# Kernel tuning notes

Hardware: AMD Instinct MI355X
Metric: run time of the kernel (lower is better)

The kernel has to match this reference:

```python
import jax, jax.numpy as jnp
import numpy as np

NUM_HEAD = 2
KR = 3          # kernel_range = [3, 3]
SHIFT = 1
N_P = KR * KR   # 9 taps
PAD = (KR // 2) * SHIFT  # 1
OFFSETS = [(i, j) for i in (-(KR // 2), 0, KR // 2) if True for j in ()]  # placeholder, real list below
OFFSETS = [(i, j) for i in range(-(KR // 2), KR // 2 + 1) for j in range(-(KR // 2), KR // 2 + 1)]


def _conv3x3(x, w, b):
    # x: [B,H,W,Cin], w: [3,3,Cin,Cout] -> SAME conv + bias
    y = jax.lax.conv_general_dilated(
        x, w, window_strides=(1, 1), padding='SAME',
        dimension_numbers=('NHWC', 'HWIO', 'NHWC'))
    return y + b


def setup_inputs() -> dict:
    key = jax.random.key(0)
    B, H, W, D = 4, 128, 128, 64
    ks = jax.random.split(key, 10)
    sc = 0.05  # small init like glorot
    return {
        'x': jax.random.normal(ks[0], (B, H, W, D), jnp.float32),
        # 1x1 conv kernels stored as matrices (equiv. to (1,1,Cin,Cout))
        'K_P': jax.random.normal(ks[1], (D, D * N_P), jnp.float32) * sc,
        'V_P': jax.random.normal(ks[2], (D, D * N_P), jnp.float32) * sc,
        'Q_P': jax.random.normal(ks[3], (D, D), jnp.float32) * sc,
        'ff1_kernel': jax.random.normal(ks[4], (D, D), jnp.float32) * sc,
        'ff1_bias': jax.random.normal(ks[5], (D,), jnp.float32) * sc,
        'ff2_kernel': jax.random.normal(ks[6], (3, 3, D, 2 * D), jnp.float32) * sc,
        'ff2_bias': jax.random.normal(ks[7], (2 * D,), jnp.float32) * sc,
        'ff3_kernel': jax.random.normal(ks[8], (3, 3, 2 * D, D), jnp.float32) * sc,
        'ff3_bias': jax.random.normal(ks[9], (D,), jnp.float32) * sc,
    }


def reference(x, K_P, V_P, Q_P, ff1_kernel, ff1_bias, ff2_kernel, ff2_bias,
              ff3_kernel, ff3_bias):
    B, H, W, D = x.shape
    hd = D // NUM_HEAD

    # 1x1 projections; K/V produce N_P channel chunks, one per tap
    x_k = jnp.einsum('bhwd,de->bhwe', x, K_P).reshape(B, H, W, N_P, D)
    x_v = jnp.einsum('bhwd,de->bhwe', x, V_P).reshape(B, H, W, N_P, D)
    x_q = jnp.einsum('bhwd,de->bhwe', x, Q_P)

    pad5 = ((0, 0), (PAD, PAD), (PAD, PAD), (0, 0), (0, 0))
    k_pad = jnp.pad(x_k, pad5)
    v_pad = jnp.pad(x_v, pad5)

    # tap t uses channel chunk t at spatial offset OFFSETS[t]*SHIFT
    def taps(padded):
        return jnp.stack(
            [padded[:, PAD + i * SHIFT:PAD + i * SHIFT + H,
                    PAD + j * SHIFT:PAD + j * SHIFT + W, t, :]
             for t, (i, j) in enumerate(OFFSETS)], axis=3)  # [B,H,W,N_P,D]

    k_taps = taps(k_pad)
    v_taps = taps(v_pad)

    # validity mask (padded taps get score 0 before softmax, as in original)
    m_pad = jnp.pad(jnp.ones((B, H, W), x.dtype), ((0, 0), (PAD, PAD), (PAD, PAD)))
    mask = jnp.stack(
        [m_pad[:, PAD + i * SHIFT:PAD + i * SHIFT + H,
               PAD + j * SHIFT:PAD + j * SHIFT + W]
         for (i, j) in OFFSETS], axis=3)  # [B,H,W,N_P]

    kh = k_taps.reshape(B, H, W, N_P, NUM_HEAD, hd)
    vh = v_taps.reshape(B, H, W, N_P, NUM_HEAD, hd)
    qh = x_q.reshape(B, H, W, NUM_HEAD, hd)

    # scores per head over taps; masked-multiply then /3, as in original
    scores = jnp.einsum('bhwtnc,bhwnc->bhwnt', kh, qh)
    scores = scores * mask[:, :, :, None, :] / 3.0
    alpha = jax.nn.softmax(scores, axis=-1)  # over taps
    attn = jnp.einsum('bhwnt,bhwtnc->bhwnc', alpha, vh).reshape(B, H, W, D)

    # FFN: 1x1 conv -> relu -> 3x3 conv -> relu -> 3x3 conv -> relu
    t = jax.nn.relu(jnp.einsum('bhwd,de->bhwe', attn, ff1_kernel) + ff1_bias)
    t = jax.nn.relu(_conv3x3(t, ff2_kernel, ff2_bias))
    t = jax.nn.relu(_conv3x3(t, ff3_kernel, ff3_bias))
    return t
```

## Files before the change

### kernel.cpp

```cpp
#include <hip/hip_runtime.h>


typedef _Float16 half8 __attribute__((ext_vector_type(8)));
typedef float f32x4 __attribute__((ext_vector_type(4)));

#define PLANE 524288

__device__ __forceinline__ f32x4 mfma16(half8 a, half8 b, f32x4 c) {
  return __builtin_amdgcn_mfma_f32_16x16x32_f16(a, b, c, 0, 0, 0);
}
__device__ __forceinline__ half8 ldfrag(const _Float16* p) { return *(const half8*)p; }
__device__ __forceinline__ half8 zfrag() { half8 z = {}; return z; }

__device__ __forceinline__ void gload_lds16(const _Float16* g, _Float16* l) {
  __builtin_amdgcn_global_load_lds(
      (const __attribute__((address_space(1))) void*)g,
      (__attribute__((address_space(3))) void*)l, 16, 0, 0);
}

__global__ __launch_bounds__(256) void prep(
    const float* __restrict__ x, const float* __restrict__ Kp,
    const float* __restrict__ Vp, const float* __restrict__ Qp,
    const float* __restrict__ W1, const float* __restrict__ F2,
    const float* __restrict__ F3, _Float16* __restrict__ xh,
    _Float16* __restrict__ out) {
  if (blockIdx.x < 2048) {
    const int t = threadIdx.x;
    const int px = blockIdx.x * 32 + (t >> 3);
    const int oct = t & 7;
    const float4* s = (const float4*)(x + (size_t)px * 64 + oct * 8);
    float4 a = s[0], b = s[1];
    half8 h = { (_Float16)a.x, (_Float16)a.y, (_Float16)a.z, (_Float16)a.w,
                (_Float16)b.x, (_Float16)b.y, (_Float16)b.z, (_Float16)b.w };
    *(half8*)(xh + (size_t)oct * PLANE + (size_t)px * 8) = h;
    return;
  }
  int e = (blockIdx.x - 2048) * 256 + threadIdx.x;
  int j = e & 7, l = (e >> 3) & 63, f = e >> 9;
  int l15 = l & 15, q8 = (l >> 4) * 8;
  float v;
  if (f < 8)        { int mb = f >> 1, kb = f & 1;
                      v = Qp[(kb*32 + q8 + j) * 64 + mb*16 + l15]; }
  else if (f < 80)  { int g = f - 8, t = g >> 3, mb = (g >> 1) & 3, kb = g & 1;
                      v = Kp[(kb*32 + q8 + j) * 576 + t*64 + mb*16 + l15]; }
  else if (f < 152) { int g = f - 80, t = g >> 3, kb = (g >> 2) & 1, nb = g & 3;
                      v = Vp[(kb*32 + q8 + j) * 576 + t*64 + nb*16 + l15]; }
  else if (f < 160) { int g = f - 152, kb = g >> 2, nb = g & 3;
                      v = W1[(kb*32 + q8 + j) * 64 + nb*16 + l15]; }
  else if (f < 304) { int g = f - 160, t = g >> 4, kb = (g >> 3) & 1, nb = g & 7;
                      v = F2[(t*64 + kb*32 + q8 + j) * 128 + nb*16 + l15]; }
  else              { int g = f - 304, t = g >> 4, kb = (g >> 2) & 3, nb = g & 3;
                      v = F3[(t*128 + kb*32 + q8 + j) * 64 + nb*16 + l15]; }
  out[e] = (_Float16)v;
}

__global__ __launch_bounds__(512) void attn_ff1(
    const _Float16* __restrict__ xh, const _Float16* __restrict__ wf,
    const float* __restrict__ f1b, _Float16* __restrict__ t1g) {
  extern __shared__ _Float16 smem[];
  const int lane = threadIdx.x & 63, wid = threadIdx.x >> 6;
  const int l15 = lane & 15, q8 = (lane >> 4) * 8;
  const int row = blockIdx.x * 2 + (wid >> 2);
  const int rw = wid & 3;
  const int p0 = row * 128 + rw * 32;
  const int h = row & 127;
  const int w0 = rw * 32;
  const int oct0 = lane >> 4;
  float* dent = (float*)(smem + 77824) + wid * 64;

  {
    const _Float16* gw = wf + 4096 + (size_t)(wid * 19) * 512;
    _Float16* lw = smem + wid * 19 * 512;
    for (int i = 0; i < 19; ++i)
      gload_lds16(gw + i * 512 + lane * 8, lw + i * 512);
  }

  half8 ax0[2], ax1[2];
#pragma unroll
  for (int m = 0; m < 2; ++m) {
    const size_t px = (size_t)(p0 + m * 16 + l15);
    ax0[m] = ldfrag(xh + (size_t)oct0 * PLANE + px * 8);
    ax1[m] = ldfrag(xh + (size_t)(oct0 + 4) * PLANE + px * 8);
  }
  f32x4 qT[2][4];
#pragma unroll
  for (int cb = 0; cb < 4; ++cb) {
    half8 aq0 = ldfrag(wf + (cb * 2 + 0) * 512 + lane * 8);
    half8 aq1 = ldfrag(wf + (cb * 2 + 1) * 512 + lane * 8);
#pragma unroll
    for (int m = 0; m < 2; ++m) {
      f32x4 c = {};
      c = mfma16(aq0, ax0[m], c);
      c = mfma16(aq1, ax1[m], c);
      qT[m][cb] = c;
    }
  }

  auto load_tap = [&](int t, half8 (&x0)[2], half8 (&x1)[2]) {
    const int dh = t / 3 - 1, dw = t % 3 - 1;
    const bool rk = (unsigned)(h + dh) < 128u;
#pragma unroll
    for (int m = 0; m < 2; ++m) {
      const bool cv = rk && ((unsigned)(w0 + m * 16 + l15 + dw) < 128u);
      const size_t px = (size_t)(p0 + m * 16 + l15 + dh * 128 + dw);
      x0[m] = cv ? ldfrag(xh + (size_t)oct0 * PLANE + px * 8) : zfrag();
      x1[m] = cv ? ldfrag(xh + (size_t)(oct0 + 4) * PLANE + px * 8) : zfrag();
    }
  };

  float den0[2] = {0.f, 0.f}, den1[2] = {0.f, 0.f};
  auto score_tap = [&](int t, half8 (&x0)[2], half8 (&x1)[2],
                       float (&e0)[2], float (&e1)[2]) {
    const int dh = t / 3 - 1;
    const bool rowok = (unsigned)(h + dh) < 128u;
    half8 kf[8];
    if (rowok) {
#pragma unroll
      for (int f = 0; f < 8; ++f)
        kf[f] = ldfrag(smem + (t * 8 + f) * 512 + lane * 8);
    }
#pragma unroll
    for (int m = 0; m < 2; ++m) {
      float pa = 0.f, pb = 0.f;
      if (rowok) {
#pragma unroll
        for (int cb = 0; cb < 4; ++cb) {
          f32x4 c = {};
          c = mfma16(kf[cb * 2 + 0], x0[m], c);
          c = mfma16(kf[cb * 2 + 1], x1[m], c);
          float d = qT[m][cb].x * c.x + qT[m][cb].y * c.y
                  + qT[m][cb].z * c.z + qT[m][cb].w * c.w;
          if (cb < 2) pa += d; else pb += d;
        }
        pa += __shfl_xor(pa, 16, 64); pa += __shfl_xor(pa, 32, 64);
        pb += __shfl_xor(pb, 16, 64); pb += __shfl_xor(pb, 32, 64);
      }
      e0[m] = __expf(pa * (1.f / 3.f));
      e1[m] = __expf(pb * (1.f / 3.f));
      den0[m] += e0[m]; den1[m] += e1[m];
    }
  };

  half8 q0[4][2], q1[4][2];
  load_tap(0, q0[0], q1[0]);
  load_tap(1, q0[1], q1[1]);
  load_tap(2, q0[2], q1[2]);

  __syncthreads();

  float e0c[2], e1c[2];
  score_tap(0, q0[0], q1[0], e0c, e1c);

  const _Float16* BVl = smem + 36864;
  f32x4 at[2][4];
#pragma unroll
  for (int m = 0; m < 2; ++m)
#pragma unroll
    for (int nb = 0; nb < 4; ++nb) at[m][nb] = f32x4{};

#pragma unroll
  for (int t = 0; t < 9; ++t) {
    if (t + 3 < 9) load_tap(t + 3, q0[(t + 3) & 3], q1[(t + 3) & 3]);
    const bool rowok = (unsigned)(h + (t / 3 - 1)) < 128u;
    if (rowok) {
      half8 vf[8];
#pragma unroll
      for (int f = 0; f < 8; ++f) vf[f] = ldfrag(BVl + (t * 8 + f) * 512 + lane * 8);
#pragma unroll
      for (int m = 0; m < 2; ++m) {
        _Float16 h0 = (_Float16)e0c[m], h1 = (_Float16)e1c[m];
        half8 b0 = {h0, h0, h0, h0, h0, h0, h0, h0};
        half8 b1 = {h1, h1, h1, h1, h1, h1, h1, h1};
        half8 s00 = q0[t & 3][m] * b0, s01 = q1[t & 3][m] * b0;
        half8 s10 = q0[t & 3][m] * b1, s11 = q1[t & 3][m] * b1;
#pragma unroll
        for (int nb = 0; nb < 2; ++nb) {
          at[m][nb]     = mfma16(s00, vf[0 * 4 + nb],     at[m][nb]);
          at[m][nb]     = mfma16(s01, vf[1 * 4 + nb],     at[m][nb]);
          at[m][nb + 2] = mfma16(s10, vf[0 * 4 + nb + 2], at[m][nb + 2]);
          at[m][nb + 2] = mfma16(s11, vf[1 * 4 + nb + 2], at[m][nb + 2]);
        }
      }
    }
    if (t < 8) {
      float e0n[2], e1n[2];
      score_tap(t + 1, q0[(t + 1) & 3], q1[(t + 1) & 3], e0n, e1n);
#pragma unroll
      for (int m = 0; m < 2; ++m) { e0c[m] = e0n[m]; e1c[m] = e1n[m]; }
    }
  }

#pragma unroll
  for (int m = 0; m < 2; ++m) {
    dent[(m * 2 + 0) * 16 + l15] = den0[m];
    dent[(m * 2 + 1) * 16 + l15] = den1[m];
  }
  f32x4 iv[2][2];
#pragma unroll
  for (int m = 0; m < 2; ++m)
#pragma unroll
    for (int hd = 0; hd < 2; ++hd) {
      f32x4 dv = *(const f32x4*)(dent + (m * 2 + hd) * 16 + (lane >> 4) * 4);
      iv[m][hd] = f32x4{1.f / dv.x, 1.f / dv.y, 1.f / dv.z, 1.f / dv.w};
    }

  __syncthreads();
  _Float16* myt = smem + wid * 2304;
#pragma unroll
  for (int m = 0; m < 2; ++m)
#pragma unroll
    for (int nb = 0; nb < 4; ++nb) {
      const int hd = nb >> 1;
#pragma unroll
      for (int r = 0; r < 4; ++r)
        myt[m * 1152 + ((lane >> 4) * 4 + r) * 72 + nb * 16 + l15] =
            (_Float16)(at[m][nb][r] * iv[m][hd][r]);
    }
  const _Float16* B1l = smem + 73728;
  const int pxl = lane >> 2;
  const int co0 = lane & 3;
#pragma unroll
  for (int m = 0; m < 2; ++m) {
    _Float16* T = myt + m * 1152;
    half8 aa0 = ldfrag(T + l15 * 72 + q8);
    half8 aa1 = ldfrag(T + l15 * 72 + 32 + q8);
#pragma unroll
    for (int nb = 0; nb < 4; ++nb) {
      f32x4 c = {};
      c = mfma16(aa0, ldfrag(B1l + (0 * 4 + nb) * 512 + lane * 8), c);
      c = mfma16(aa1, ldfrag(B1l + (1 * 4 + nb) * 512 + lane * 8), c);
      float bv = f1b[nb * 16 + l15];
#pragma unroll
      for (int r = 0; r < 4; ++r)
        T[((lane >> 4) * 4 + r) * 72 + nb * 16 + l15] =
            (_Float16)fmaxf(c[r] + bv, 0.f);
    }
    const size_t pxg = (size_t)(p0 + m * 16 + pxl);
    half8 h0 = ldfrag(T + pxl * 72 + co0 * 8);
    half8 h1 = ldfrag(T + pxl * 72 + (co0 + 4) * 8);
    *(half8*)(t1g + (size_t)co0 * PLANE + pxg * 8) = h0;
    *(half8*)(t1g + (size_t)(co0 + 4) * PLANE + pxg * 8) = h1;
  }
}

template <int KB, int NBL, int COUT, int DEPTH>
__global__ __launch_bounds__(512, 4) void conv3x3(
    const _Float16* __restrict__ in, const _Float16* __restrict__ wfrag,
    const float* __restrict__ bias, void* __restrict__ outp, int out_fp32) {
  extern __shared__ _Float16 smem[];
  constexpr int NS = DEPTH + 1;
  const int lane = threadIdx.x & 63, wid = threadIdx.x >> 6;
  const int l15 = lane & 15;
  const int nh = blockIdx.x & 1;
  const int pairIdx = blockIdx.x >> 1;
  const int row = pairIdx * 2 + (wid >> 2);
  const int rw = wid & 3;
  const int p0 = row * 128 + rw * 32;
  const int h = row & 127;
  const int w0 = rw * 32;
  const int NBF = COUT / 16;
  const int oct0 = lane >> 4;

  {
    for (int s = 0; s < 9; ++s) {
      int f = wid * 9 + s;
      int t = f >> 3, r = f & 7, kb = r / NBL, i = r % NBL;
      const _Float16* g = wfrag + (size_t)((t * KB + kb) * NBF + nh * NBL + i) * 512;
      gload_lds16(g + lane * 8, smem + f * 512);
    }
  }

  f32x4 acc[2][NBL];
#pragma unroll
  for (int m = 0; m < 2; ++m)
#pragma unroll
    for (int nb = 0; nb < NBL; ++nb) acc[m][nb] = f32x4{};

  auto load_conv = [&](int t, half8 (&dst)[2][KB]) {
    const int dh = t / 3 - 1, dw = t % 3 - 1;
    const bool rk = (unsigned)(h + dh) < 128u;
#pragma unroll
    for (int m = 0; m < 2; ++m) {
      const bool cv = rk && ((unsigned)(w0 + m * 16 + l15 + dw) < 128u);
      const size_t px = (size_t)(p0 + m * 16 + l15 + dh * 128 + dw);
#pragma unroll
      for (int kb = 0; kb < KB; ++kb)
        dst[m][kb] = cv ? ldfrag(in + (size_t)(kb * 4 + oct0) * PLANE + px * 8) : zfrag();
    }
  };

  half8 aq[NS][2][KB];
#pragma unroll
  for (int d = 0; d < DEPTH; ++d) load_conv(d, aq[d]);

  __syncthreads();

#pragma unroll
  for (int t = 0; t < 9; ++t) {
    if (t + DEPTH < 9) load_conv(t + DEPTH, aq[(t + DEPTH) % NS]);
    const bool rowok = (unsigned)(h + (t / 3 - 1)) < 128u;
    if (rowok) {
#pragma unroll
      for (int nb = 0; nb < NBL; ++nb) {
#pragma unroll
        for (int kb = 0; kb < KB; ++kb) {
          half8 b = ldfrag(smem + (size_t)((t * KB + kb) * NBL + nb) * 512 + lane * 8);
          acc[0][nb] = mfma16(aq[t % NS][0][kb], b, acc[0][nb]);
          acc[1][nb] = mfma16(aq[t % NS][1][kb], b, acc[1][nb]);
        }
      }
    }
  }

  if (out_fp32) {
#pragma unroll
    for (int m = 0; m < 2; ++m)
#pragma unroll
      for (int nb = 0; nb < NBL; ++nb) {
        const int ch = nh * NBL * 16 + nb * 16 + l15;
        float bv = bias[ch];
#pragma unroll
        for (int r = 0; r < 4; ++r) {
          float v = fmaxf(acc[m][nb][r] + bv, 0.f);
          size_t px = (size_t)(p0 + m * 16 + (lane >> 4) * 4 + r);
          ((float*)outp)[px * COUT + ch] = v;
        }
      }
  } else {
    __syncthreads();
    _Float16* T = smem + wid * 1152;
    const int pxl = lane >> 2, co0 = lane & 3;
#pragma unroll
    for (int m = 0; m < 2; ++m) {
#pragma unroll
      for (int nb = 0; nb < NBL; ++nb) {
        const int chl = nb * 16 + l15;
        float bv = bias[nh * NBL * 16 + chl];
#pragma unroll
        for (int r = 0; r < 4; ++r)
          T[((lane >> 4) * 4 + r) * 72 + chl] =
              (_Float16)fmaxf(acc[m][nb][r] + bv, 0.f);
      }
      const size_t pxg = (size_t)(p0 + m * 16 + pxl);
      half8 h0 = ldfrag(T + pxl * 72 + co0 * 8);
      half8 h1 = ldfrag(T + pxl * 72 + (co0 + 4) * 8);
      *(half8*)((_Float16*)outp + (size_t)(nh * 8 + co0) * PLANE + pxg * 8) = h0;
      *(half8*)((_Float16*)outp + (size_t)(nh * 8 + co0 + 4) * PLANE + pxg * 8) = h1;
    }
  }
}

extern "C" void kernel_launch(void* const* d_in, const int* in_sizes, int n_in,
                              void* d_out, int out_size, void* d_ws, size_t ws_size,
                              hipStream_t stream) {
  (void)in_sizes; (void)n_in; (void)out_size; (void)ws_size;
  const float* x   = (const float*)d_in[0];
  const float* Kp  = (const float*)d_in[1];
  const float* Vp  = (const float*)d_in[2];
  const float* Qp  = (const float*)d_in[3];
  const float* f1w = (const float*)d_in[4];
  const float* f1b = (const float*)d_in[5];
  const float* f2w = (const float*)d_in[6];
  const float* f2b = (const float*)d_in[7];
  const float* f3w = (const float*)d_in[8];
  const float* f3b = (const float*)d_in[9];

  _Float16* xh  = (_Float16*)d_ws;
  _Float16* wf  = xh + 4194304;
  _Float16* t1g = wf + 229376;
  _Float16* t2g = t1g + 4194304;
  float* outp = (float*)d_out;

  (void)hipFuncSetAttribute((const void*)attn_ff1,
      hipFuncAttributeMaxDynamicSharedMemorySize, 157696);
  (void)hipFuncSetAttribute((const void*)conv3x3<2, 4, 128, 3>,
      hipFuncAttributeMaxDynamicSharedMemorySize, 73728);
  (void)hipFuncSetAttribute((const void*)conv3x3<4, 2, 64, 1>,
      hipFuncAttributeMaxDynamicSharedMemorySize, 73728);

  prep<<<2944, 256, 0, stream>>>(x, Kp, Vp, Qp, f1w, f2w, f3w, xh, wf);
  attn_ff1<<<256, 512, 157696, stream>>>(xh, wf, f1b, t1g);
  conv3x3<2, 4, 128, 3><<<512, 512, 73728, stream>>>(t1g, wf + 81920, f2b, t2g, 0);
  conv3x3<4, 2, 64, 1><<<512, 512, 73728, stream>>>(t2g, wf + 155648, f3b, outp, 1);
}
```

Before: 137.7 us.

## Deepen attention tap prefetch and replace final conv with split-K-half kernel

The attention kernel now prefetches four taps ahead with a five-slot register ring instead of three ahead with four slots, to hide more global-load latency. The last 3x3 conv is replaced by a dedicated kernel that processes input channels in two halves, keeping a three-deep activation prefetch ring and weights staged in LDS. It writes fp32 output directly per lane without the LDS transpose. The deeper prefetch raises register pressure, and the new store pattern is less coalesced.

```diff
diff --git a/kernel.cpp b/kernel.cpp
--- a/kernel.cpp
+++ b/kernel.cpp
@@ -141,10 +141,11 @@
     }
   };
 
-  half8 q0[4][2], q1[4][2];
+  half8 q0[5][2], q1[5][2];
   load_tap(0, q0[0], q1[0]);
   load_tap(1, q0[1], q1[1]);
   load_tap(2, q0[2], q1[2]);
+  load_tap(3, q0[3], q1[3]);
 
   __syncthreads();
 
@@ -160,7 +161,7 @@
 
 #pragma unroll
   for (int t = 0; t < 9; ++t) {
-    if (t + 3 < 9) load_tap(t + 3, q0[(t + 3) & 3], q1[(t + 3) & 3]);
+    if (t + 4 < 9) load_tap(t + 4, q0[(t + 4) % 5], q1[(t + 4) % 5]);
     const bool rowok = (unsigned)(h + (t / 3 - 1)) < 128u;
     if (rowok) {
       half8 vf[8];
@@ -171,8 +172,8 @@
         _Float16 h0 = (_Float16)e0c[m], h1 = (_Float16)e1c[m];
         half8 b0 = {h0, h0, h0, h0, h0, h0, h0, h0};
         half8 b1 = {h1, h1, h1, h1, h1, h1, h1, h1};
-        half8 s00 = q0[t & 3][m] * b0, s01 = q1[t & 3][m] * b0;
-        half8 s10 = q0[t & 3][m] * b1, s11 = q1[t & 3][m] * b1;
+        half8 s00 = q0[t % 5][m] * b0, s01 = q1[t % 5][m] * b0;
+        half8 s10 = q0[t % 5][m] * b1, s11 = q1[t % 5][m] * b1;
 #pragma unroll
         for (int nb = 0; nb < 2; ++nb) {
           at[m][nb]     = mfma16(s00, vf[0 * 4 + nb],     at[m][nb]);
@@ -184,7 +185,7 @@
     }
     if (t < 8) {
       float e0n[2], e1n[2];
-      score_tap(t + 1, q0[(t + 1) & 3], q1[(t + 1) & 3], e0n, e1n);
+      score_tap(t + 1, q0[(t + 1) % 5], q1[(t + 1) % 5], e0n, e1n);
 #pragma unroll
       for (int m = 0; m < 2; ++m) { e0c[m] = e0n[m]; e1c[m] = e1n[m]; }
     }
@@ -350,6 +351,93 @@
   }
 }
 
+__global__ __launch_bounds__(512, 4) void conv3b(
+    const _Float16* __restrict__ in, const _Float16* __restrict__ wfrag,
+    const float* __restrict__ bias, float* __restrict__ outp) {
+  extern __shared__ _Float16 smem[];
+  const int lane = threadIdx.x & 63, wid = threadIdx.x >> 6;
+  const int l15 = lane & 15;
+  const int nh = blockIdx.x & 1;
+  const int pairIdx = blockIdx.x >> 1;
+  const int row = pairIdx * 2 + (wid >> 2);
+  const int rw = wid & 3;
+  const int p0 = row * 128 + rw * 32;
+  const int h = row & 127;
+  const int w0 = rw * 32;
+  const int oct0 = lane >> 4;
+  const int KB = 4, NBL = 2, NBF = 4, COUT = 64;
+
+  {
+    for (int s = 0; s < 9; ++s) {
+      int f = wid * 9 + s;
+      int t = f >> 3, r = f & 7, kb = r / NBL, i = r % NBL;
+      const _Float16* g = wfrag + (size_t)((t * KB + kb) * NBF + nh * NBL + i) * 512;
+      gload_lds16(g + lane * 8, smem + f * 512);
+    }
+  }
+
+  f32x4 acc[2][2];
+#pragma unroll
+  for (int m = 0; m < 2; ++m)
+#pragma unroll
+    for (int nb = 0; nb < 2; ++nb) acc[m][nb] = f32x4{};
+
+#pragma unroll
+  for (int p = 0; p < 2; ++p) {
+    auto load_half = [&](int t, half8 (&dst)[2][2]) {
+      const int dh = t / 3 - 1, dw = t % 3 - 1;
+      const bool rk = (unsigned)(h + dh) < 128u;
+#pragma unroll
+      for (int m = 0; m < 2; ++m) {
+        const bool cv = rk && ((unsigned)(w0 + m * 16 + l15 + dw) < 128u);
+        const size_t px = (size_t)(p0 + m * 16 + l15 + dh * 128 + dw);
+#pragma unroll
+        for (int kbl = 0; kbl < 2; ++kbl)
+          dst[m][kbl] = cv
+              ? ldfrag(in + (size_t)((2 * p + kbl) * 4 + oct0) * PLANE + px * 8)
+              : zfrag();
+      }
+    };
+
+    half8 aq[3][2][2];
+    load_half(0, aq[0]);
+    load_half(1, aq[1]);
+    if (p == 0) __syncthreads();
+
+#pragma unroll
+    for (int t = 0; t < 9; ++t) {
+      if (t + 2 < 9) load_half(t + 2, aq[(t + 2) % 3]);
+      const bool rowok = (unsigned)(h + (t / 3 - 1)) < 128u;
+      if (rowok) {
+#pragma unroll
+        for (int nb = 0; nb < 2; ++nb) {
+#pragma unroll
+          for (int kbl = 0; kbl < 2; ++kbl) {
+            half8 b = ldfrag(smem +
+                (size_t)((t * KB + 2 * p + kbl) * NBL + nb) * 512 + lane * 8);
+            acc[0][nb] = mfma16(aq[t % 3][0][kbl], b, acc[0][nb]);
+            acc[1][nb] = mfma16(aq[t % 3][1][kbl], b, acc[1][nb]);
+          }
+        }
+      }
+    }
+  }
+
+#pragma unroll
+  for (int m = 0; m < 2; ++m)
+#pragma unroll
+    for (int nb = 0; nb < 2; ++nb) {
+      const int ch = nh * 32 + nb * 16 + l15;
+      float bv = bias[ch];
+#pragma unroll
+      for (int r = 0; r < 4; ++r) {
+        float v = fmaxf(acc[m][nb][r] + bv, 0.f);
+        size_t px = (size_t)(p0 + m * 16 + (lane >> 4) * 4 + r);
+        outp[px * COUT + ch] = v;
+      }
+    }
+}
+
 extern "C" void kernel_launch(void* const* d_in, const int* in_sizes, int n_in,
                               void* d_out, int out_size, void* d_ws, size_t ws_size,
                               hipStream_t stream) {
@@ -375,11 +463,11 @@
       hipFuncAttributeMaxDynamicSharedMemorySize, 157696);
   (void)hipFuncSetAttribute((const void*)conv3x3<2, 4, 128, 3>,
       hipFuncAttributeMaxDynamicSharedMemorySize, 73728);
-  (void)hipFuncSetAttribute((const void*)conv3x3<4, 2, 64, 1>,
+  (void)hipFuncSetAttribute((const void*)conv3b,
       hipFuncAttributeMaxDynamicSharedMemorySize, 73728);
 
   prep<<<2944, 256, 0, stream>>>(x, Kp, Vp, Qp, f1w, f2w, f3w, xh, wf);
   attn_ff1<<<256, 512, 157696, stream>>>(xh, wf, f1b, t1g);
   conv3x3<2, 4, 128, 3><<<512, 512, 73728, stream>>>(t1g, wf + 81920, f2b, t2g, 0);
-  conv3x3<4, 2, 64, 1><<<512, 512, 73728, stream>>>(t2g, wf + 155648, f3b, outp, 1);
-}
+  conv3b<<<512, 512, 73728, stream>>>(t2g, wf + 155648, f3b, outp);
+}
```

Result: no change. 136.7 us (-0.8%).
